# Optimization experiments

Hardware: AMD Instinct MI355X
Metric: run time of the kernel (lower is better)

## Reference

```python
import jax, jax.numpy as jnp
import numpy as np
import math

B, N, H = 2, 2048, 16
D_NOPE, D_ROPE, D_V = 128, 64, 128
Q_HEAD_DIM = D_NOPE + D_ROPE  # 192
HID, QR, KVR = 2048, 1536, 512
THETA = 10000.0
EPS = 1e-6


def _rmsnorm(x, w):
    var = jnp.mean(jnp.square(x.astype(jnp.float32)), axis=-1, keepdims=True)
    return w * (x * jax.lax.rsqrt(var + EPS)).astype(x.dtype)


def _permute_pairs(x):
    # torch: view(..., d//2, 2).transpose(-1,-2).reshape(..., d)
    # -> concat(evens, odds) along last dim
    return jnp.concatenate([x[..., 0::2], x[..., 1::2]], axis=-1)


def _rotate_half(x):
    x1, x2 = x[..., : x.shape[-1] // 2], x[..., x.shape[-1] // 2:]
    return jnp.concatenate([-x2, x1], axis=-1)


def _rope_tables(pos_ids):
    inv_freq = 1.0 / (THETA ** (jnp.arange(0, D_ROPE, 2, dtype=jnp.float32) / D_ROPE))
    t = jnp.arange(N, dtype=jnp.float32)
    freqs = jnp.outer(t, inv_freq)                 # [N, 32]
    emb = jnp.concatenate([freqs, freqs], axis=-1) # [N, 64]
    cos = jnp.cos(emb)[pos_ids][:, None]           # [B, 1, N, 64]
    sin = jnp.sin(emb)[pos_ids][:, None]
    return cos, sin


def mla_forward(x, Wq_down, q_norm_w, Wq_up, Wkv_down, kv_norm_w, Wkv_up, Wo, mask, pos_ids):
    b, n, _ = x.shape
    # low-rank Q path
    q = _rmsnorm(x @ Wq_down, q_norm_w) @ Wq_up          # [B, N, H*192]
    q = q.reshape(b, n, H, Q_HEAD_DIM).transpose(0, 2, 1, 3)  # [B, H, N, 192]
    q_nope, q_pe = q[..., :D_NOPE], q[..., D_NOPE:]
    # low-rank KV path
    kv = x @ Wkv_down                                    # [B, N, 512+64]
    kv_c, k_pe = kv[..., :KVR], kv[..., KVR:]
    k_pe = k_pe.reshape(b, n, 1, D_ROPE).transpose(0, 2, 1, 3)  # [B, 1, N, 64]
    kv_up = _rmsnorm(kv_c, kv_norm_w) @ Wkv_up           # [B, N, H*256]
    kv_up = kv_up.reshape(b, n, H, D_NOPE + D_V).transpose(0, 2, 1, 3)  # [B, H, N, 256]
    k_nope, v = kv_up[..., :D_NOPE], kv_up[..., D_NOPE:]
    # partial RoPE (with the pair-permute quirk from the torch code)
    cos, sin = _rope_tables(pos_ids)
    q_pe = _permute_pairs(q_pe)
    k_pe = _permute_pairs(k_pe)
    q_pe = q_pe * cos + _rotate_half(q_pe) * sin
    k_pe = k_pe * cos + _rotate_half(k_pe) * sin
    q_full = jnp.concatenate([q_nope, q_pe], axis=-1)                       # [B, H, N, 192]
    k_full = jnp.concatenate([k_nope, jnp.broadcast_to(k_pe, (b, H, n, D_ROPE))], axis=-1)
    scores = jnp.einsum('bhqd,bhkd->bhqk', q_full, k_full) / math.sqrt(Q_HEAD_DIM)
    scores = jnp.where(mask == 0, -jnp.inf, scores)
    attn = jax.nn.softmax(scores.astype(jnp.float32), axis=-1)
    out = jnp.einsum('bhqk,bhkd->bhqd', attn, v)          # [B, H, N, 128]
    out = out.transpose(0, 2, 1, 3).reshape(b, n, H * D_V)
    return out @ Wo


def setup_inputs() -> dict:
    key = jax.random.key(0)
    ks = jax.random.split(key, 7)
    s = 0.02
    return {
        'x': jax.random.normal(ks[0], (B, N, HID), jnp.float32),
        'Wq_down': jax.random.normal(ks[1], (HID, QR), jnp.float32) * s,
        'q_norm_w': jnp.ones((QR,), jnp.float32),
        'Wq_up': jax.random.normal(ks[2], (QR, H * Q_HEAD_DIM), jnp.float32) * s,
        'Wkv_down': jax.random.normal(ks[3], (HID, KVR + D_ROPE), jnp.float32) * s,
        'kv_norm_w': jnp.ones((KVR,), jnp.float32),
        'Wkv_up': jax.random.normal(ks[4], (KVR, H * (D_NOPE + D_V)), jnp.float32) * s,
        'Wo': jax.random.normal(ks[5], (H * D_V, HID), jnp.float32) * s,
        'mask': jnp.ones((1, 1, N, N), jnp.bool_),
        'pos_ids': jnp.broadcast_to(jnp.arange(N, dtype=jnp.int32), (B, N)),
    }


def reference(x, Wq_down, q_norm_w, Wq_up, Wkv_down, kv_norm_w, Wkv_up, Wo, mask, pos_ids):
    return mla_forward(x, Wq_down, q_norm_w, Wq_up, Wkv_down, kv_norm_w, Wkv_up, Wo, mask, pos_ids)
```

## Files before the change

kernel.cpp:

```cpp
#include <hip/hip_runtime.h>
#include <hip/hip_bf16.h>
#include <cstdint>

#define B_ 2
#define N_ 2048
#define H_ 16
#define HID_ 2048
#define QR_ 1536
#define KVR_ 512
#define DN_ 128
#define DR_ 64
#define DV_ 128
#define QHD_ 192

typedef __attribute__((ext_vector_type(8))) short short8;
typedef __attribute__((ext_vector_type(4))) float f32x4;

union bfu { __hip_bfloat16 b; short s; };

static __device__ __forceinline__ void bf_split(float v, short& hi, short& lo) {
  bfu uh, ul;
  uh.b = __float2bfloat16(v);
  float hf = __bfloat162float(uh.b);
  ul.b = __float2bfloat16(v - hf);
  hi = uh.s; lo = ul.s;
}

static __device__ __forceinline__ void gload16(const void* g, void* l) {
  __builtin_amdgcn_global_load_lds(
      (const __attribute__((address_space(1))) uint32_t*)(g),
      (__attribute__((address_space(3))) uint32_t*)(l), 16, 0, 0);
}


__global__ __launch_bounds__(256) void conv_a_kernel(
    const float* __restrict__ A, uint8_t* __restrict__ img, int K, int nks, int total) {
  int gid = blockIdx.x * 256 + threadIdx.x;
  if (gid >= total) return;
  int perRow = K >> 3;
  int row = gid / perRow, kc = (gid - row * perRow) << 3;
  const float* src = A + (size_t)row * K + kc;
  short8 hi, lo;
#pragma unroll
  for (int j = 0; j < 8; ++j) { short a, b; bf_split(src[j], a, b); hi[j] = a; lo[j] = b; }
  int mb = row >> 7, r = row & 127, sw = (r & 7) << 4;
  uint8_t* base = img + ((size_t)mb * nks << 14) + r * 128;
  auto put = [&](int p, short8 v) {
    int ks = p >> 6, s = (p >> 3) & 7;
    *(short8*)(base + ((size_t)ks << 14) + ((16 * s) ^ sw)) = v;
  };
  put(kc, hi); put(K + kc, lo); put(2 * K + kc, hi);
}

__global__ __launch_bounds__(256) void conv_b_kernel(
    const float* __restrict__ Bw, uint8_t* __restrict__ img, int K, int N,
    int Npad, int nbase, int nks, int total) {
  int gid = blockIdx.x * 256 + threadIdx.x;
  if (gid >= total) return;
  int perN = K >> 3;
  int n = gid / perN, kc = (gid - n * perN) << 3;
  short8 hi = {0,0,0,0,0,0,0,0}, lo = {0,0,0,0,0,0,0,0};
  if (n < N) {
#pragma unroll
    for (int j = 0; j < 8; ++j) {
      short a, b; bf_split(Bw[(size_t)(kc + j) * N + n], a, b); hi[j] = a; lo[j] = b;
    }
  }
  int nn = nbase * 128 + n;
  int nb = nn >> 7, r = nn & 127, sw = (r & 7) << 4;
  uint8_t* base = img + ((size_t)nb * nks << 14) + r * 128;
  auto put = [&](int p, short8 v) {
    int ks = p >> 6, s = (p >> 3) & 7;
    *(short8*)(base + ((size_t)ks << 14) + ((16 * s) ^ sw)) = v;
  };
  put(kc, hi); put(K + kc, hi); put(2 * K + kc, lo);
}

__global__ __launch_bounds__(256) void rmsnorm_img_kernel(
    const float* __restrict__ in, const float* __restrict__ w,
    uint8_t* __restrict__ img, int len, int istride, int nks) {
  __shared__ float red[4];
  const int row = blockIdx.x;
  const float* x = in + (size_t)row * istride;
  float ss = 0.f;
  for (int i = threadIdx.x; i < len; i += 256) { float v = x[i]; ss += v * v; }
#pragma unroll
  for (int o = 32; o > 0; o >>= 1) ss += __shfl_down(ss, o, 64);
  if ((threadIdx.x & 63) == 0) red[threadIdx.x >> 6] = ss;
  __syncthreads();
  if (threadIdx.x == 0)
    red[0] = rsqrtf((red[0] + red[1] + red[2] + red[3]) / (float)len + 1e-6f);
  __syncthreads();
  const float inv = red[0];
  int mb = row >> 7, r = row & 127, sw = (r & 7) << 4;
  uint8_t* base = img + ((size_t)mb * nks << 14) + r * 128;
  auto put = [&](int p, short8 v) {
    int ks = p >> 6, s = (p >> 3) & 7;
    *(short8*)(base + ((size_t)ks << 14) + ((16 * s) ^ sw)) = v;
  };
  for (int kc = threadIdx.x * 8; kc < len; kc += 2048) {
    short8 hi, lo;
#pragma unroll
    for (int j = 0; j < 8; ++j) {
      short a, b; bf_split(w[kc + j] * (x[kc + j] * inv), a, b); hi[j] = a; lo[j] = b;
    }
    put(kc, hi); put(len + kc, lo); put(2 * len + kc, hi);
  }
}

__global__ __launch_bounds__(256) void gemm_bf16_kernel(
    const uint8_t* __restrict__ Aimg, const uint8_t* __restrict__ Bimg,
    float* __restrict__ C, int N, int nks) {
  __shared__ __align__(16) uint8_t As[16384];
  __shared__ __align__(16) uint8_t Bs[16384];
  const int tid = threadIdx.x;
  const int lane = tid & 63;
  const int wave = tid >> 6;
  const int wm = wave >> 1, wn = wave & 1;
  const int lr = lane & 15, g = lane >> 4;
  const int mb = blockIdx.y, nb = blockIdx.x;
  const uint8_t* ga = Aimg + ((size_t)mb * nks << 14);
  const uint8_t* gb = Bimg + ((size_t)nb * nks << 14);

  f32x4 acc[4][4];
#pragma unroll
  for (int i = 0; i < 4; ++i)
#pragma unroll
    for (int j = 0; j < 4; ++j) acc[i][j] = (f32x4){0.f, 0.f, 0.f, 0.f};

  for (int ks = 0; ks < nks; ++ks) {
    __syncthreads();
#pragma unroll
    for (int i = 0; i < 4; ++i)
      gload16(ga + ((size_t)ks << 14) + (wave * 4 + i) * 1024 + lane * 16,
              As + (wave * 4 + i) * 1024);
#pragma unroll
    for (int i = 0; i < 4; ++i)
      gload16(gb + ((size_t)ks << 14) + (wave * 4 + i) * 1024 + lane * 16,
              Bs + (wave * 4 + i) * 1024);
    __syncthreads();
#pragma unroll
    for (int c = 0; c < 2; ++c) {
      short8 af[4], bf[4];
#pragma unroll
      for (int i = 0; i < 4; ++i) {
        int ar = wm * 64 + i * 16 + lr;
        af[i] = *(const short8*)(As + ar * 128 + ((16 * (c * 4 + g)) ^ ((ar & 7) << 4)));
        int br = wn * 64 + i * 16 + lr;
        bf[i] = *(const short8*)(Bs + br * 128 + ((16 * (c * 4 + g)) ^ ((br & 7) << 4)));
      }
#pragma unroll
      for (int i = 0; i < 4; ++i)
#pragma unroll
        for (int j = 0; j < 4; ++j)
          acc[i][j] = __builtin_amdgcn_mfma_f32_16x16x32_bf16(af[i], bf[j], acc[i][j], 0, 0, 0);
    }
  }
#pragma unroll
  for (int i = 0; i < 4; ++i)
#pragma unroll
    for (int q = 0; q < 4; ++q) {
      float* rp = C + (size_t)(mb * 128 + wm * 64 + i * 16 + g * 4 + q) * N +
                  nb * 128 + wn * 64 + lr;
#pragma unroll
      for (int j = 0; j < 4; ++j) rp[j * 16] = acc[i][j][q];
    }
}

__global__ __launch_bounds__(256) void conv_kn_kernel(
    const float* __restrict__ kv_up, uint8_t* __restrict__ Kn) {
  const int kt = blockIdx.x, bh = blockIdx.y;
  const int b = bh >> 4, h = bh & 15;
  uint8_t* tile = Kn + (((size_t)bh * 64 + kt) << 14);
  for (int f = threadIdx.x; f < 512; f += 256) {
    int r = f >> 4, s = f & 15;
    int tok = b * N_ + kt * 32 + r;
    const float* src = kv_up + (size_t)tok * 4096 + h * 256 + s * 8;
    short8 hi, lo;
#pragma unroll
    for (int j = 0; j < 8; ++j) { short a, bq; bf_split(src[j], a, bq); hi[j] = a; lo[j] = bq; }
    int sw = (r & 7) << 4;
    *(short8*)(tile + r * 512 + ((16 * s) ^ sw)) = hi;
    *(short8*)(tile + r * 512 + ((16 * (s + 16)) ^ sw)) = lo;
  }
}

__global__ __launch_bounds__(256) void conv_v_kernel(
    const float* __restrict__ kv_up, uint8_t* __restrict__ Vimg) {
  const int kt = blockIdx.x, bh = blockIdx.y;
  const int b = bh >> 4, h = bh & 15;
  uint8_t* tile = Vimg + (((size_t)bh * 64 + kt) << 14);
  for (int f = threadIdx.x; f < 512; f += 256) {
    int d = f >> 2, gg = f & 3;
    int tok0 = b * N_ + kt * 32 + gg * 8;
    short8 hi, lo;
#pragma unroll
    for (int j = 0; j < 8; ++j) {
      short a, bq;
      bf_split(kv_up[(size_t)(tok0 + j) * 4096 + h * 256 + 128 + d], a, bq);
      hi[j] = a; lo[j] = bq;
    }
    int sw = (d & 7) << 4;
    *(short8*)(tile + d * 128 + ((16 * gg) ^ sw)) = hi;
    *(short8*)(tile + d * 128 + ((16 * (4 + gg)) ^ sw)) = lo;
  }
}

__device__ __forceinline__ void rope_apply(const float* __restrict__ src,
                                           float* __restrict__ dst, float pos) {
  float xv[64];
#pragma unroll
  for (int i = 0; i < 64; ++i) xv[i] = src[i];
#pragma unroll
  for (int i = 0; i < 32; ++i) {
    float freq = __expf(-0.2878231366f * (float)i);
    float s, c;
    sincosf(pos * freq, &s, &c);
    dst[i]      = xv[2 * i] * c - xv[2 * i + 1] * s;
    dst[i + 32] = xv[2 * i + 1] * c + xv[2 * i] * s;
  }
}

__global__ __launch_bounds__(256) void rope_q_kernel(float* __restrict__ q,
                                                     const int* __restrict__ pos_ids) {
  int idx = blockIdx.x * 256 + threadIdx.x;
  if (idx >= B_ * N_ * H_) return;
  int t = idx >> 4, h = idx & 15;
  float* p = q + (size_t)t * (H_ * QHD_) + h * QHD_ + DN_;
  rope_apply(p, p, (float)pos_ids[t]);
}

__global__ __launch_bounds__(256) void rope_k_kernel(const float* __restrict__ Cmat,
                                                     const int* __restrict__ pos_ids,
                                                     uint8_t* __restrict__ Kp) {
  int t = blockIdx.x * 256 + threadIdx.x;
  if (t >= B_ * N_) return;
  float rv[64];
  rope_apply(Cmat + (size_t)t * 2176 + 2048, rv, (float)pos_ids[t]);
  int b = t >> 11, tt = t & 2047, kt = tt >> 5, r = tt & 31;
  uint8_t* tp = Kp + (((size_t)b * 64 + kt) << 13) + r * 256;
  int sw = (r & 7) << 4;
#pragma unroll
  for (int s = 0; s < 8; ++s) {
    short8 hi, lo;
#pragma unroll
    for (int j = 0; j < 8; ++j) { short a, bq; bf_split(rv[s * 8 + j], a, bq); hi[j] = a; lo[j] = bq; }
    *(short8*)(tp + ((16 * s) ^ sw)) = hi;
    *(short8*)(tp + ((16 * (s + 8)) ^ sw)) = lo;
  }
}

__global__ __launch_bounds__(256, 2) void attn_mfma_kernel(
    const float* __restrict__ q_up,
    const uint8_t* __restrict__ Kn, const uint8_t* __restrict__ Kp,
    const uint8_t* __restrict__ Vv,
    float* __restrict__ aout) {
  __shared__ __align__(16) uint8_t Ksn[32 * 512];
  __shared__ __align__(16) uint8_t Ksp[32 * 256];
  __shared__ __align__(16) uint8_t Vs[128 * 128];
  __shared__ __align__(16) uint8_t Ps[4 * 4096];

  const int tid = threadIdx.x;
  const int lane = tid & 63;
  const int wave = tid >> 6;
  const int g = lane >> 4;
  const int lr = lane & 15;
  const int bh = blockIdx.y;
  const int b = bh >> 4, h = bh & 15;
  const int q0 = blockIdx.x << 7;

  short8 qhi[2][6], qlo[2][6];
  {
    const float scale = 0.07216878364870323f;
#pragma unroll
    for (int tl = 0; tl < 2; ++tl) {
      const int tok = b * N_ + q0 + wave * 32 + tl * 16 + lr;
      const float* qp = q_up + (size_t)tok * (H_ * QHD_) + h * QHD_;
#pragma unroll
      for (int c = 0; c < 6; ++c) {
        const float* src = qp + c * 32 + g * 8;
#pragma unroll
        for (int j = 0; j < 8; ++j) {
          short a, bq; bf_split(src[j] * scale, a, bq);
          qhi[tl][c][j] = a; qlo[tl][c][j] = bq;
        }
      }
    }
  }

  f32x4 acc_o[2][8];
#pragma unroll
  for (int tl = 0; tl < 2; ++tl)
#pragma unroll
    for (int i = 0; i < 8; ++i) acc_o[tl][i] = (f32x4){0.f, 0.f, 0.f, 0.f};
  float m_r[2][4], l_r[2][4];
#pragma unroll
  for (int tl = 0; tl < 2; ++tl)
#pragma unroll
    for (int j = 0; j < 4; ++j) { m_r[tl][j] = -1e30f; l_r[tl][j] = 0.f; }

  for (int kt = 0; kt < N_ / 32; ++kt) {
    __syncthreads();
    {
      const uint8_t* gkn = Kn + (((size_t)bh * 64 + kt) << 14);
      const uint8_t* gkp = Kp + (((size_t)b * 64 + kt) << 13);
      const uint8_t* gv  = Vv + (((size_t)bh * 64 + kt) << 14);
#pragma unroll
      for (int i = 0; i < 4; ++i)
        gload16(gkn + (wave * 4 + i) * 1024 + lane * 16, Ksn + (wave * 4 + i) * 1024);
#pragma unroll
      for (int i = 0; i < 2; ++i)
        gload16(gkp + (wave * 2 + i) * 1024 + lane * 16, Ksp + (wave * 2 + i) * 1024);
#pragma unroll
      for (int i = 0; i < 4; ++i)
        gload16(gv + (wave * 4 + i) * 1024 + lane * 16, Vs + (wave * 4 + i) * 1024);
    }
    __syncthreads();

    f32x4 accs[2][2];
#pragma unroll
    for (int t = 0; t < 2; ++t) {
      f32x4 aA = {0.f, 0.f, 0.f, 0.f};
      f32x4 aB = {0.f, 0.f, 0.f, 0.f};
      const int krow = t * 16 + lr;
      const int sw = (krow & 7) << 4;
      const uint8_t* kb = Ksn + krow * 512;
#pragma unroll
      for (int c = 0; c < 4; ++c) {
        short8 kh = *(const short8*)(kb + ((16 * (c * 4 + g)) ^ sw));
        short8 kl = *(const short8*)(kb + ((16 * (c * 4 + g + 16)) ^ sw));
        aA = __builtin_amdgcn_mfma_f32_16x16x32_bf16(qhi[0][c], kh, aA, 0, 0, 0);
        aA = __builtin_amdgcn_mfma_f32_16x16x32_bf16(qhi[0][c], kl, aA, 0, 0, 0);
        aA = __builtin_amdgcn_mfma_f32_16x16x32_bf16(qlo[0][c], kh, aA, 0, 0, 0);
        aB = __builtin_amdgcn_mfma_f32_16x16x32_bf16(qhi[1][c], kh, aB, 0, 0, 0);
        aB = __builtin_amdgcn_mfma_f32_16x16x32_bf16(qhi[1][c], kl, aB, 0, 0, 0);
        aB = __builtin_amdgcn_mfma_f32_16x16x32_bf16(qlo[1][c], kh, aB, 0, 0, 0);
      }
      const uint8_t* pb = Ksp + krow * 256;
#pragma unroll
      for (int c2 = 0; c2 < 2; ++c2) {
        short8 kh = *(const short8*)(pb + ((16 * (c2 * 4 + g)) ^ sw));
        short8 kl = *(const short8*)(pb + ((16 * (c2 * 4 + g + 8)) ^ sw));
        aA = __builtin_amdgcn_mfma_f32_16x16x32_bf16(qhi[0][4 + c2], kh, aA, 0, 0, 0);
        aA = __builtin_amdgcn_mfma_f32_16x16x32_bf16(qhi[0][4 + c2], kl, aA, 0, 0, 0);
        aA = __builtin_amdgcn_mfma_f32_16x16x32_bf16(qlo[0][4 + c2], kh, aA, 0, 0, 0);
        aB = __builtin_amdgcn_mfma_f32_16x16x32_bf16(qhi[1][4 + c2], kh, aB, 0, 0, 0);
        aB = __builtin_amdgcn_mfma_f32_16x16x32_bf16(qhi[1][4 + c2], kl, aB, 0, 0, 0);
        aB = __builtin_amdgcn_mfma_f32_16x16x32_bf16(qlo[1][4 + c2], kh, aB, 0, 0, 0);
      }
      accs[0][t] = aA; accs[1][t] = aB;
    }

    float fac[2][4], p0[2][4], p1[2][4];
#pragma unroll
    for (int tl = 0; tl < 2; ++tl)
#pragma unroll
      for (int j = 0; j < 4; ++j) {
        float rm = fmaxf(accs[tl][0][j], accs[tl][1][j]);
        rm = fmaxf(rm, __shfl_xor(rm, 1, 64));
        rm = fmaxf(rm, __shfl_xor(rm, 2, 64));
        rm = fmaxf(rm, __shfl_xor(rm, 4, 64));
        rm = fmaxf(rm, __shfl_xor(rm, 8, 64));
        float mn = fmaxf(m_r[tl][j], rm);
        fac[tl][j] = __expf(m_r[tl][j] - mn);
        m_r[tl][j] = mn;
        p0[tl][j] = __expf(accs[tl][0][j] - mn);
        p1[tl][j] = __expf(accs[tl][1][j] - mn);
        float rs = p0[tl][j] + p1[tl][j];
        rs += __shfl_xor(rs, 1, 64);
        rs += __shfl_xor(rs, 2, 64);
        rs += __shfl_xor(rs, 4, 64);
        rs += __shfl_xor(rs, 8, 64);
        l_r[tl][j] = l_r[tl][j] * fac[tl][j] + rs;
      }
#pragma unroll
    for (int tl = 0; tl < 2; ++tl)
#pragma unroll
      for (int dt = 0; dt < 8; ++dt)
#pragma unroll
        for (int j = 0; j < 4; ++j) acc_o[tl][dt][j] *= fac[tl][j];

#pragma unroll
    for (int tl = 0; tl < 2; ++tl) {
      uint8_t* pw = Ps + wave * 4096 + tl * 2048;
#pragma unroll
      for (int j = 0; j < 4; ++j) {
        int r = g * 4 + j;
        int rsw = (r & 7) << 4;
        uint8_t* rowp = pw + r * 128;
#pragma unroll
        for (int t = 0; t < 2; ++t) {
          float p = t ? p1[tl][j] : p0[tl][j];
          int k = t * 16 + lr;
          short a, bq; bf_split(p, a, bq);
          *(short*)(rowp + ((((k >> 3) + 0) * 16) ^ rsw) + (k & 7) * 2) = a;
          *(short*)(rowp + ((((k >> 3) + 4) * 16) ^ rsw) + (k & 7) * 2) = bq;
        }
      }
    }

    {
      const uint8_t* prA = Ps + wave * 4096 + lr * 128;
      const uint8_t* prB = prA + 2048;
      const int psw = (lr & 7) << 4;
      short8 phA = *(const short8*)(prA + ((16 * g) ^ psw));
      short8 plA = *(const short8*)(prA + ((16 * (4 + g)) ^ psw));
      short8 phB = *(const short8*)(prB + ((16 * g) ^ psw));
      short8 plB = *(const short8*)(prB + ((16 * (4 + g)) ^ psw));
#pragma unroll
      for (int dt = 0; dt < 8; ++dt) {
        int dcol = dt * 16 + lr;
        const uint8_t* vb = Vs + dcol * 128;
        int vsw = (dcol & 7) << 4;
        short8 vh = *(const short8*)(vb + ((16 * g) ^ vsw));
        short8 vl = *(const short8*)(vb + ((16 * (4 + g)) ^ vsw));
        acc_o[0][dt] = __builtin_amdgcn_mfma_f32_16x16x32_bf16(phA, vh, acc_o[0][dt], 0, 0, 0);
        acc_o[0][dt] = __builtin_amdgcn_mfma_f32_16x16x32_bf16(phA, vl, acc_o[0][dt], 0, 0, 0);
        acc_o[0][dt] = __builtin_amdgcn_mfma_f32_16x16x32_bf16(plA, vh, acc_o[0][dt], 0, 0, 0);
        acc_o[1][dt] = __builtin_amdgcn_mfma_f32_16x16x32_bf16(phB, vh, acc_o[1][dt], 0, 0, 0);
        acc_o[1][dt] = __builtin_amdgcn_mfma_f32_16x16x32_bf16(phB, vl, acc_o[1][dt], 0, 0, 0);
        acc_o[1][dt] = __builtin_amdgcn_mfma_f32_16x16x32_bf16(plB, vh, acc_o[1][dt], 0, 0, 0);
      }
    }
  }

#pragma unroll
  for (int tl = 0; tl < 2; ++tl) {
    float inv[4];
#pragma unroll
    for (int j = 0; j < 4; ++j) inv[j] = 1.f / l_r[tl][j];
    const int tokb = b * N_ + q0 + wave * 32 + tl * 16 + g * 4;
#pragma unroll
    for (int j = 0; j < 4; ++j) {
      float* orow = aout + (size_t)(tokb + j) * (H_ * DV_) + h * DV_;
#pragma unroll
      for (int dt = 0; dt < 8; ++dt)
        orow[dt * 16 + lr] = acc_o[tl][dt][j] * inv[j];
    }
  }
}

extern "C" void kernel_launch(void* const* d_in, const int* in_sizes, int n_in,
                              void* d_out, int out_size, void* d_ws, size_t ws_size,
                              hipStream_t stream) {
  (void)in_sizes; (void)n_in; (void)out_size; (void)ws_size;
  const float* x         = (const float*)d_in[0];
  const float* Wq_down   = (const float*)d_in[1];
  const float* q_norm_w  = (const float*)d_in[2];
  const float* Wq_up     = (const float*)d_in[3];
  const float* Wkv_down  = (const float*)d_in[4];
  const float* kv_norm_w = (const float*)d_in[5];
  const float* Wkv_up    = (const float*)d_in[6];
  const float* Wo        = (const float*)d_in[7];
  const int* pos_ids     = (const int*)d_in[9];
  float* out = (float*)d_out;

  uint8_t* W = (uint8_t*)d_ws;
  uint8_t* Xi    = W;
  uint8_t* Bslot = W + 50331648;
  float*   qtkv  = (float*)(W + 79691776);
  float*   q_up  = (float*)(W + 115343360);
  uint8_t* Kpimg = W + 165675008;
  uint8_t* KvAimg= W + 67108864;
  uint8_t* WkvBimg=W + 79691776;
  float*   kv_up = (float*)(W + 0);
  uint8_t* Knimg = W + 67108864;
  float*   a_out = (float*)(W + 0);
  uint8_t* A2img = W + 33554432;
  uint8_t* Woimg = W + 100663296;
  uint8_t* Vimg  = (uint8_t*)d_out;

  dim3 blk(256);
  conv_a_kernel<<<4096, blk, 0, stream>>>(x, Xi, 2048, 96, 4096 * 256);
  conv_b_kernel<<<1536, blk, 0, stream>>>(Wq_down, Bslot, 2048, 1536, 1536, 0, 96, 1536 * 256);
  conv_b_kernel<<<640, blk, 0, stream>>>(Wkv_down, Bslot, 2048, 576, 640, 12, 96, 640 * 256);
  gemm_bf16_kernel<<<dim3(17, 32), blk, 0, stream>>>(Xi, Bslot, qtkv, 2176, 96);
  rmsnorm_img_kernel<<<4096, blk, 0, stream>>>(qtkv, q_norm_w, Xi, 1536, 2176, 72);
  conv_b_kernel<<<2304, blk, 0, stream>>>(Wq_up, Bslot, 1536, 3072, 3072, 0, 72, 2304 * 256);
  gemm_bf16_kernel<<<dim3(24, 32), blk, 0, stream>>>(Xi, Bslot, q_up, 3072, 72);
  rope_q_kernel<<<256, blk, 0, stream>>>(q_up, pos_ids);
  rope_k_kernel<<<16, blk, 0, stream>>>(qtkv, pos_ids, Kpimg);
  rmsnorm_img_kernel<<<4096, blk, 0, stream>>>(qtkv + 1536, kv_norm_w, KvAimg, 512, 2176, 24);
  conv_b_kernel<<<1024, blk, 0, stream>>>(Wkv_up, WkvBimg, 512, 4096, 4096, 0, 24, 1024 * 256);
  gemm_bf16_kernel<<<dim3(32, 32), blk, 0, stream>>>(KvAimg, WkvBimg, kv_up, 4096, 24);
  conv_kn_kernel<<<dim3(64, 32), blk, 0, stream>>>(kv_up, Knimg);
  conv_v_kernel<<<dim3(64, 32), blk, 0, stream>>>(kv_up, Vimg);
  attn_mfma_kernel<<<dim3(16, 32), blk, 0, stream>>>(q_up, Knimg, Kpimg, Vimg, a_out);
  conv_a_kernel<<<4096, blk, 0, stream>>>(a_out, A2img, 2048, 96, 4096 * 256);
  conv_b_kernel<<<2048, blk, 0, stream>>>(Wo, Woimg, 2048, 2048, 2048, 0, 96, 2048 * 256);
  gemm_bf16_kernel<<<dim3(16, 32), blk, 0, stream>>>(A2img, Woimg, out, 2048, 96);
}
```

Measured before the change: 1.169 ms.

## Double-buffer K-nope tiles and stagger K/V prefetch in attention loop

Restructures the attention key loop so the next tile's K-nope is prefetched into a second LDS buffer while the current QK MFMAs run. K-rope and V loads are issued as soon as their buffers are free, and explicit vmcnt/lgkmcnt waits with barriers replace the two full __syncthreads. This is meant to hide global-to-LDS latency behind compute. It also raises wave priority around the MFMA blocks with s_setprio. The cost is extra LDS for the second K buffer and more fragile hand-counted wait logic.

Result: slower. 1.205 ms (+3.0%).

```diff
diff --git a/kernel.cpp b/kernel.cpp
--- a/kernel.cpp
+++ b/kernel.cpp
@@ -31,6 +31,22 @@
       (const __attribute__((address_space(1))) uint32_t*)(g),
       (__attribute__((address_space(3))) uint32_t*)(l), 16, 0, 0);
 }
+
+#define VM_BARRIER(N)                                   \
+  do {                                                  \
+    asm volatile("s_waitcnt vmcnt(" #N ")" ::: "memory"); \
+    __builtin_amdgcn_sched_barrier(0);                  \
+    __builtin_amdgcn_s_barrier();                       \
+    __builtin_amdgcn_sched_barrier(0);                  \
+  } while (0)
+
+#define LGKM_BARRIER()                                  \
+  do {                                                  \
+    asm volatile("s_waitcnt lgkmcnt(0)" ::: "memory");  \
+    __builtin_amdgcn_sched_barrier(0);                  \
+    __builtin_amdgcn_s_barrier();                       \
+    __builtin_amdgcn_sched_barrier(0);                  \
+  } while (0)
 
 
 __global__ __launch_bounds__(256) void conv_a_kernel(
@@ -255,7 +271,7 @@
     const uint8_t* __restrict__ Kn, const uint8_t* __restrict__ Kp,
     const uint8_t* __restrict__ Vv,
     float* __restrict__ aout) {
-  __shared__ __align__(16) uint8_t Ksn[32 * 512];
+  __shared__ __align__(16) uint8_t Ksn[2][32 * 512];
   __shared__ __align__(16) uint8_t Ksp[32 * 256];
   __shared__ __align__(16) uint8_t Vs[128 * 128];
   __shared__ __align__(16) uint8_t Ps[4 * 4096];
@@ -299,32 +315,47 @@
 #pragma unroll
     for (int j = 0; j < 4; ++j) { m_r[tl][j] = -1e30f; l_r[tl][j] = 0.f; }
 
+  const size_t knbase = ((size_t)bh * 64) << 14;
+  const size_t kpbase = ((size_t)b * 64) << 13;
+  const size_t vbase  = ((size_t)bh * 64) << 14;
+
+  {
+    const uint8_t* gkn = Kn + knbase;
+    const uint8_t* gkp = Kp + kpbase;
+    const uint8_t* gv  = Vv + vbase;
+#pragma unroll
+    for (int i = 0; i < 4; ++i)
+      gload16(gkn + (wave * 4 + i) * 1024 + lane * 16, Ksn[0] + (wave * 4 + i) * 1024);
+#pragma unroll
+    for (int i = 0; i < 2; ++i)
+      gload16(gkp + (wave * 2 + i) * 1024 + lane * 16, Ksp + (wave * 2 + i) * 1024);
+#pragma unroll
+    for (int i = 0; i < 4; ++i)
+      gload16(gv + (wave * 4 + i) * 1024 + lane * 16, Vs + (wave * 4 + i) * 1024);
+  }
+  VM_BARRIER(4);
+
+  int cbuf = 0;
   for (int kt = 0; kt < N_ / 32; ++kt) {
-    __syncthreads();
+    const int ktn = (kt + 1 < N_ / 32) ? kt + 1 : kt;
+
     {
-      const uint8_t* gkn = Kn + (((size_t)bh * 64 + kt) << 14);
-      const uint8_t* gkp = Kp + (((size_t)b * 64 + kt) << 13);
-      const uint8_t* gv  = Vv + (((size_t)bh * 64 + kt) << 14);
+      const uint8_t* gkn = Kn + knbase + ((size_t)ktn << 14);
 #pragma unroll
       for (int i = 0; i < 4; ++i)
-        gload16(gkn + (wave * 4 + i) * 1024 + lane * 16, Ksn + (wave * 4 + i) * 1024);
-#pragma unroll
-      for (int i = 0; i < 2; ++i)
-        gload16(gkp + (wave * 2 + i) * 1024 + lane * 16, Ksp + (wave * 2 + i) * 1024);
-#pragma unroll
-      for (int i = 0; i < 4; ++i)
-        gload16(gv + (wave * 4 + i) * 1024 + lane * 16, Vs + (wave * 4 + i) * 1024);
-    }
-    __syncthreads();
+        gload16(gkn + (wave * 4 + i) * 1024 + lane * 16,
+                Ksn[cbuf ^ 1] + (wave * 4 + i) * 1024);
+    }
 
     f32x4 accs[2][2];
+    __builtin_amdgcn_s_setprio(1);
 #pragma unroll
     for (int t = 0; t < 2; ++t) {
       f32x4 aA = {0.f, 0.f, 0.f, 0.f};
       f32x4 aB = {0.f, 0.f, 0.f, 0.f};
       const int krow = t * 16 + lr;
       const int sw = (krow & 7) << 4;
-      const uint8_t* kb = Ksn + krow * 512;
+      const uint8_t* kb = Ksn[cbuf] + krow * 512;
 #pragma unroll
       for (int c = 0; c < 4; ++c) {
         short8 kh = *(const short8*)(kb + ((16 * (c * 4 + g)) ^ sw));
@@ -350,6 +381,7 @@
       }
       accs[0][t] = aA; accs[1][t] = aB;
     }
+    __builtin_amdgcn_s_setprio(0);
 
     float fac[2][4], p0[2][4], p1[2][4];
 #pragma unroll
@@ -380,6 +412,15 @@
 #pragma unroll
         for (int j = 0; j < 4; ++j) acc_o[tl][dt][j] *= fac[tl][j];
 
+    VM_BARRIER(4);
+
+    {
+      const uint8_t* gkp = Kp + kpbase + ((size_t)ktn << 13);
+#pragma unroll
+      for (int i = 0; i < 2; ++i)
+        gload16(gkp + (wave * 2 + i) * 1024 + lane * 16, Ksp + (wave * 2 + i) * 1024);
+    }
+
 #pragma unroll
     for (int tl = 0; tl < 2; ++tl) {
       uint8_t* pw = Ps + wave * 4096 + tl * 2048;
@@ -407,6 +448,7 @@
       short8 plA = *(const short8*)(prA + ((16 * (4 + g)) ^ psw));
       short8 phB = *(const short8*)(prB + ((16 * g) ^ psw));
       short8 plB = *(const short8*)(prB + ((16 * (4 + g)) ^ psw));
+      __builtin_amdgcn_s_setprio(1);
 #pragma unroll
       for (int dt = 0; dt < 8; ++dt) {
         int dcol = dt * 16 + lr;
@@ -421,7 +463,20 @@
         acc_o[1][dt] = __builtin_amdgcn_mfma_f32_16x16x32_bf16(phB, vl, acc_o[1][dt], 0, 0, 0);
         acc_o[1][dt] = __builtin_amdgcn_mfma_f32_16x16x32_bf16(plB, vh, acc_o[1][dt], 0, 0, 0);
       }
-    }
+      __builtin_amdgcn_s_setprio(0);
+    }
+
+    LGKM_BARRIER();
+
+    {
+      const uint8_t* gv = Vv + vbase + ((size_t)ktn << 14);
+#pragma unroll
+      for (int i = 0; i < 4; ++i)
+        gload16(gv + (wave * 4 + i) * 1024 + lane * 16, Vs + (wave * 4 + i) * 1024);
+    }
+
+    VM_BARRIER(4);
+    cbuf ^= 1;
   }
 
 #pragma unroll
```
